# Optimization experiments

Hardware: AMD Instinct MI355X
Metric: run time of the kernel (lower is better)

Reference implementation:

```python
import jax, jax.numpy as jnp
import numpy as np

N_BINS = 256
HOP = 80


def _gru(xs, Wih, Whh, bih, bhh, reverse=False):
    """Single-layer unidirectional GRU, PyTorch gate layout (r, z, n).
    xs: (T, B, I); Wih: (3H, I); Whh: (3H, H). Returns (T, B, H)."""
    H = Whh.shape[1]
    gi = jnp.einsum('tbi,gi->tbg', xs, Wih) + bih  # precompute input projections

    def step(h, gi_t):
        gh = h @ Whh.T + bhh
        ir, iz, inn = jnp.split(gi_t, 3, axis=-1)
        hr, hz, hn = jnp.split(gh, 3, axis=-1)
        r = jax.nn.sigmoid(ir + hr)
        z = jax.nn.sigmoid(iz + hz)
        n = jnp.tanh(inn + r * hn)
        h_new = (1.0 - z) * n + z * h
        return h_new, h_new

    h0 = jnp.zeros((xs.shape[1], H), xs.dtype)
    _, ys = jax.lax.scan(step, h0, gi, reverse=reverse)
    return ys


def _quantize(w):
    # continuous [-1, 1] -> bin index in [0, N_BINS-1]
    return jnp.clip(jnp.floor((w + 1.0) * (N_BINS / 2)), 0, N_BINS - 1).astype(jnp.int32)


def _forward(x, y, p):
    # --- encode: 2-layer bidirectional GRU over mel frames ---
    c = x
    for l in ('m0', 'm1'):
        f = _gru(c, p[l + 'f_Wih'], p[l + 'f_Whh'], p[l + 'f_bih'], p[l + 'f_bhh'])
        bwd = _gru(c, p[l + 'b_Wih'], p[l + 'b_Whh'], p[l + 'b_bih'], p[l + 'b_bhh'], reverse=True)
        c = jnp.concatenate([f, bwd], axis=-1)  # (t_m, b, 2*dim_enc)
    # nearest-neighbor upsample in time (matches F.interpolate default 'nearest')
    c = jnp.repeat(c, HOP, axis=0)  # (t_w, b, 2*dim_enc)

    # --- teacher forcing: shift waveform right, vectorize via embedding ---
    b = x.shape[1]
    w = jnp.concatenate([jnp.zeros((1, b), y.dtype), y[:-1]], axis=0)
    e = p['E'][_quantize(w)]  # (t_w, b, dim_vec)

    # --- wav GRU + projection + GELU ---
    o = _gru(jnp.concatenate([e, c], axis=-1), p['w_Wih'], p['w_Whh'], p['w_bih'], p['w_bhh'])
    o = jax.nn.gelu(o @ p['Wp'].T + p['bp'], approximate=False)  # (t_w, b, dim_proj)

    # --- categorical neg log prob over quantized targets ---
    logits = o @ p['Wd'].T + p['bd']  # (t_w, b, N_BINS)
    logp = jax.nn.log_softmax(logits, axis=-1)
    tgt = _quantize(y)
    nll = -jnp.mean(jnp.take_along_axis(logp, tgt[..., None], axis=-1))
    return nll


def setup_inputs() -> dict:
    key = jax.random.key(0)
    ks = iter(jax.random.split(key, 64))

    def rn(shape, s=0.08):
        return jax.random.normal(next(ks), shape, jnp.float32) * s

    t_m, b, dm = 32, 4, 80
    de, dv, dd, dp = 128, 256, 896, 512
    d = {}
    d['x'] = jax.random.normal(next(ks), (t_m, b, dm), jnp.float32)
    d['y'] = jax.random.uniform(next(ks), (t_m * HOP, b), jnp.float32, minval=-1.0, maxval=1.0)
    for name, i in [('m0f', dm), ('m0b', dm), ('m1f', 2 * de), ('m1b', 2 * de)]:
        d[name + '_Wih'] = rn((3 * de, i))
        d[name + '_Whh'] = rn((3 * de, de))
        d[name + '_bih'] = rn((3 * de,))
        d[name + '_bhh'] = rn((3 * de,))
    d['w_Wih'] = rn((3 * dd, 2 * de + dv))
    d['w_Whh'] = rn((3 * dd, dd))
    d['w_bih'] = rn((3 * dd,))
    d['w_bhh'] = rn((3 * dd,))
    d['Wp'] = rn((dp, dd))
    d['bp'] = rn((dp,))
    d['E'] = rn((N_BINS, dv))
    d['Wd'] = rn((N_BINS, dp))
    d['bd'] = rn((N_BINS,))
    return d


def reference(x, y, m0f_Wih, m0f_Whh, m0f_bih, m0f_bhh, m0b_Wih, m0b_Whh, m0b_bih, m0b_bhh,
              m1f_Wih, m1f_Whh, m1f_bih, m1f_bhh, m1b_Wih, m1b_Whh, m1b_bih, m1b_bhh,
              w_Wih, w_Whh, w_bih, w_bhh, Wp, bp, E, Wd, bd):
    p = dict(m0f_Wih=m0f_Wih, m0f_Whh=m0f_Whh, m0f_bih=m0f_bih, m0f_bhh=m0f_bhh,
             m0b_Wih=m0b_Wih, m0b_Whh=m0b_Whh, m0b_bih=m0b_bih, m0b_bhh=m0b_bhh,
             m1f_Wih=m1f_Wih, m1f_Whh=m1f_Whh, m1f_bih=m1f_bih, m1f_bhh=m1f_bhh,
             m1b_Wih=m1b_Wih, m1b_Whh=m1b_Whh, m1b_bih=m1b_bih, m1b_bhh=m1b_bhh,
             w_Wih=w_Wih, w_Whh=w_Whh, w_bih=w_bih, w_bhh=w_bhh,
             Wp=Wp, bp=bp, E=E, Wd=Wd, bd=bd)
    return _forward(x, y, p)
```

## Files before the change

### kernel.cpp

```cpp
#include <hip/hip_runtime.h>
#include <stdint.h>
#include <math.h>

typedef __attribute__((ext_vector_type(8))) short bf16x8;
typedef __attribute__((ext_vector_type(4))) float f32x4;
typedef __attribute__((ext_vector_type(4))) unsigned int u32x4;

#define BATCH 4
#define T_M 32
#define DE 128
#define T_W 2560
#define NWG 56

__device__ __forceinline__ float b2f(unsigned short h) {
  return __uint_as_float(((unsigned int)h) << 16);
}
__device__ __forceinline__ unsigned short f2b(float f) {
  unsigned int u = __float_as_uint(f);
  u = u + 0x7fffu + ((u >> 16) & 1u);
  return (unsigned short)(u >> 16);
}
__device__ __forceinline__ float blo(unsigned int u){ return __uint_as_float(u << 16); }
__device__ __forceinline__ float bhi(unsigned int u){ return __uint_as_float(u & 0xffff0000u); }
__device__ __forceinline__ float sigm(float x){
  return __builtin_amdgcn_rcpf(1.f + __expf(-x));
}
__device__ __forceinline__ float tanh_fast(float x){
  float x2 = fminf(fmaxf(x + x, -30.f), 30.f);
  return 1.f - 2.f * __builtin_amdgcn_rcpf(__expf(x2) + 1.f);
}
__device__ __forceinline__ float gelu_exact(float x){ return 0.5f * x * (1.f + erff(x * 0.70710678118654752f)); }

__global__ __launch_bounds__(256) void k_prep(
    const float* __restrict__ wih, const float* __restrict__ wp,
    const float* __restrict__ wd, const float* __restrict__ e,
    const float* __restrict__ whh,
    unsigned short* __restrict__ wih_b, unsigned short* __restrict__ wp_b,
    unsigned short* __restrict__ wd_b, unsigned short* __restrict__ eb,
    unsigned short* __restrict__ whh_p)
{
  int idx = blockIdx.x * 256 + threadIdx.x;
  const int N0 = 2688 * 512, N1 = 512 * 896, N2 = 256 * 512, N3 = 256 * 256;
  if (idx < N0) { wih_b[idx] = f2b(wih[idx]); return; }
  idx -= N0;
  if (idx < N1) { wp_b[idx] = f2b(wp[idx]); return; }
  idx -= N1;
  if (idx < N2) { wd_b[idx] = f2b(wd[idx]); return; }
  idx -= N2;
  if (idx < N3) { eb[idx] = f2b(e[idx]); return; }
  idx -= N3;
  if (idx >= 224 * 28 * 512) return;
  int j    = idx & 7;
  int r16  = (idx >> 3) & 15;
  int quad = (idx >> 7) & 3;
  int kc   = (idx >> 9) % 28;
  int G    = (idx >> 9) / 28;
  unsigned short val = 0;
  if (r16 < 12) {
    int row = (r16 >> 2) * 896 + G * 4 + (r16 & 3);
    int col = kc * 32 + quad * 8 + j;
    val = f2b(whh[(size_t)row * 896 + col]);
  }
  whh_p[idx] = val;
}

__global__ __launch_bounds__(384) void k_gi_enc(
    const float* __restrict__ in, const float* __restrict__ Wih,
    const float* __restrict__ bih, float* __restrict__ out, int K)
{
  __shared__ float in_s[256];
  int tb = blockIdx.x;
  for (int i = threadIdx.x; i < K; i += 384) in_s[i] = in[tb * K + i];
  __syncthreads();
  int row = threadIdx.x;
  float acc = bih[row];
  const float* wr = Wih + row * K;
  for (int k = 0; k < K; k += 4) {
    float4 w = *(const float4*)(wr + k);
    float4 v = *(const float4*)(in_s + k);
    acc += w.x * v.x + w.y * v.y + w.z * v.z + w.w * v.w;
  }
  out[tb * 384 + row] = acc;
}

__global__ __launch_bounds__(512) void k_scan_enc(
    const float* __restrict__ gi_f, const float* __restrict__ gi_b,
    const float* __restrict__ whh_f, const float* __restrict__ bhh_f,
    const float* __restrict__ whh_b, const float* __restrict__ bhh_b,
    float* __restrict__ c_out, unsigned short* __restrict__ cb)
{
  const int dir = blockIdx.x, tid = threadIdx.x;
  const float* gi  = dir ? gi_b  : gi_f;
  const float* whh = dir ? whh_b : whh_f;
  const float* bhh = dir ? bhh_b : bhh_f;
  __shared__ unsigned short h_s[BATCH][DE + 8];
  __shared__ float gh_s[384][4];
  __shared__ float bhh_s[384];
  for (int i = tid; i < 384; i += 512) bhh_s[i] = bhh[i];
  for (int i = tid; i < BATCH * (DE + 8); i += 512) ((unsigned short*)h_s)[i] = 0;
  __syncthreads();
  for (int s = 0; s < T_M; ++s) {
    int t = dir ? (T_M - 1 - s) : s;
    #pragma unroll
    for (int k3 = 0; k3 < 3; ++k3) {
      int d = tid + 512 * k3;
      int row = d >> 2, b = d & 3;
      const float* wr = whh + row * DE;
      float acc = 0.f;
      for (int j = 0; j < DE; j += 8) {
        float4 w0 = *(const float4*)(wr + j);
        float4 w1 = *(const float4*)(wr + j + 4);
        uint4  hv = *(const uint4*)&h_s[b][j];
        acc += w0.x * blo(hv.x) + w0.y * bhi(hv.x) + w0.z * blo(hv.y) + w0.w * bhi(hv.y);
        acc += w1.x * blo(hv.z) + w1.y * bhi(hv.z) + w1.z * blo(hv.w) + w1.w * bhi(hv.w);
      }
      gh_s[row][b] = acc + bhh_s[row];
    }
    __syncthreads();
    {
      int u = tid >> 2, b = tid & 3;
      const float* git = gi + (t * BATCH + b) * 384;
      float r = sigm(git[u] + gh_s[u][b]);
      float z = sigm(git[DE + u] + gh_s[DE + u][b]);
      float n = tanh_fast(git[2 * DE + u] + r * gh_s[2 * DE + u][b]);
      float hold = b2f(h_s[b][u]);
      float hnew = (1.f - z) * n + z * hold;
      int oi = (t * BATCH + b) * 256 + dir * DE + u;
      c_out[oi] = hnew;
      if (cb) cb[oi] = f2b(hnew);
      h_s[b][u] = f2b(hnew);
    }
    __syncthreads();
  }
}

__global__ __launch_bounds__(256) void k_mgemm(
    const unsigned short* __restrict__ A, const unsigned short* __restrict__ B,
    const float* __restrict__ bias, void* __restrict__ C,
    int M, int N, int K, int act, int c_bf16, int swz, int afuse,
    const unsigned short* __restrict__ Eb, const unsigned short* __restrict__ c1b,
    const float* __restrict__ yw)
{
  __shared__ unsigned short As[128][40];
  __shared__ unsigned short Bs[128][40];
  const int tid = threadIdx.x;
  const int m0 = blockIdx.x * 128, n0 = blockIdx.y * 128;
  const int lane = tid & 63, wave = tid >> 6;
  const int wy = wave >> 1, wx = wave & 1;
  const int row16 = lane & 15, quad = lane >> 4;
  const int sr = tid >> 1, sc = (tid & 1) * 16;
  const unsigned short* arow0 = nullptr;
  const unsigned short* arow1 = nullptr;
  if (afuse) {
    int row = m0 + sr, tt = row >> 2, b = row & 3;
    float w = (tt == 0) ? 0.f : yw[(tt - 1) * 4 + b];
    int q = (int)floorf((w + 1.f) * 128.f);
    q = q < 0 ? 0 : (q > 255 ? 255 : q);
    arow0 = Eb + q * 256;
    arow1 = c1b + ((tt / 80) * 4 + b) * 256;
  }
  f32x4 acc[4][4] = {};
  for (int kt = 0; kt < K; kt += 32) {
    uint4 av, av2;
    if (afuse) {
      int kk = kt + sc;
      const unsigned short* src = (kk < 256) ? (arow0 + kk) : (arow1 + kk - 256);
      av  = *(const uint4*)src;
      av2 = *(const uint4*)(src + 8);
    } else {
      av  = *(const uint4*)(A + (size_t)(m0 + sr) * K + kt + sc);
      av2 = *(const uint4*)(A + (size_t)(m0 + sr) * K + kt + sc + 8);
    }
    uint4 bv  = *(const uint4*)(B + (size_t)(n0 + sr) * K + kt + sc);
    uint4 bv2 = *(const uint4*)(B + (size_t)(n0 + sr) * K + kt + sc + 8);
    __syncthreads();
    *(uint4*)&As[sr][sc] = av; *(uint4*)&As[sr][sc + 8] = av2;
    *(uint4*)&Bs[sr][sc] = bv; *(uint4*)&Bs[sr][sc + 8] = bv2;
    __syncthreads();
    bf16x8 af[4], bf[4];
    #pragma unroll
    for (int i = 0; i < 4; ++i) af[i] = *(const bf16x8*)&As[wy * 64 + i * 16 + row16][quad * 8];
    #pragma unroll
    for (int j = 0; j < 4; ++j) bf[j] = *(const bf16x8*)&Bs[wx * 64 + j * 16 + row16][quad * 8];
    #pragma unroll
    for (int i = 0; i < 4; ++i)
      #pragma unroll
      for (int j = 0; j < 4; ++j)
        acc[i][j] = __builtin_amdgcn_mfma_f32_16x16x32_bf16(af[i], bf[j], acc[i][j], 0, 0, 0);
  }
  #pragma unroll
  for (int i = 0; i < 4; ++i) {
    #pragma unroll
    for (int j = 0; j < 4; ++j) {
      int col = n0 + wx * 64 + j * 16 + row16;
      float bs = bias[col];
      #pragma unroll
      for (int r = 0; r < 4; ++r) {
        int row = m0 + wy * 64 + i * 16 + quad * 4 + r;
        float v = acc[i][j][r] + bs;
        if (act) v = gelu_exact(v);
        if (swz) {
          int t = row >> 2, b = row & 3;
          int g = col / 896, rem = col - g * 896;
          int G = rem >> 2, u = rem & 3;
          ((unsigned short*)C)[(size_t)(t * 224 + G) * 48 + g * 16 + b * 4 + u] = f2b(v);
        } else if (c_bf16) {
          ((unsigned short*)C)[(size_t)row * N + col] = f2b(v);
        } else {
          ((float*)C)[(size_t)row * N + col] = v;
        }
      }
    }
  }
}

__global__ __launch_bounds__(256, 1) void k_wav_rnn(
    const unsigned short* __restrict__ whh_p,
    const float* __restrict__ bhh,
    const unsigned short* __restrict__ gp_,
    unsigned int* __restrict__ hslots,
    unsigned int* __restrict__ O32)
{
  const int wg = blockIdx.x, tid = threadIdx.x;
  const int lane = tid & 63, wave = tid >> 6;
  const int G = wg * 4 + wave;

  __shared__ unsigned short h_lds[2][4][912];
  __shared__ float phh[4][3][4][4];

  const int r16 = lane & 15, quad = lane >> 4, bb = lane & 3;
  const int fu = (lane >> 2) & 3, fb = lane & 3;

  bf16x8 wf[28];
  {
    const bf16x8* W8 = (const bf16x8*)whh_p + (size_t)G * 28 * 64;
    #pragma unroll
    for (int kc = 0; kc < 28; ++kc)
      wf[kc] = W8[(kc * 4 + quad) * 16 + r16];
  }

  const float br_ = bhh[G * 4 + fu];
  const float bz_ = bhh[896 + G * 4 + fu];
  const float bn_ = bhh[1792 + G * 4 + fu];
  float hprev = 0.f;
  const unsigned short* gl0 = gp_ + (size_t)G * 48 + fb * 4 + fu;
  unsigned short cr = gl0[0], cz = gl0[16], cn = gl0[32];

  const int p0 = tid, p1 = tid + 256, p2 = tid + 512;
  const int p3 = (tid < 128) ? tid + 768 : tid;
  const int pb0 = p0 / 224, pG0 = p0 - pb0 * 224;
  const int pb1 = p1 / 224, pG1 = p1 - pb1 * 224;
  const int pb2 = p2 / 224, pG2 = p2 - pb2 * 224;
  const int pb3 = p3 / 224, pG3 = p3 - pb3 * 224;

  const unsigned long long base0 = (unsigned long long)hslots;
  const unsigned long long base1 = base0 + 14336ull;

  for (int t = 0; t < T_W; ++t) {
    const unsigned long long hb = (t & 1) ? base1 : base0;
    unsigned long long a0 = hb + ((unsigned long long)p0 << 4);
    unsigned long long a1 = hb + ((unsigned long long)p1 << 4);
    unsigned long long a2 = hb + ((unsigned long long)p2 << 4);
    unsigned long long a3 = hb + ((unsigned long long)p3 << 4);
    u32x4 s0, s1, s2, s3;
    const unsigned int tg = (unsigned int)t;
    for (;;) {
      asm volatile(
        "global_load_dwordx4 %0, %4, off sc0 sc1\n"
        "global_load_dwordx4 %1, %5, off sc0 sc1\n"
        "global_load_dwordx4 %2, %6, off sc0 sc1\n"
        "global_load_dwordx4 %3, %7, off sc0 sc1\n"
        "s_waitcnt vmcnt(0)"
        : "=&v"(s0), "=&v"(s1), "=&v"(s2), "=&v"(s3)
        : "v"(a0), "v"(a1), "v"(a2), "v"(a3)
        : "memory");
      unsigned int bad = (s0.z ^ tg) | (s1.z ^ tg) | (s2.z ^ tg) | (s3.z ^ tg);
      if (!__any(bad != 0)) break;
    }

    int tn = (t + 1 < T_W) ? (t + 1) : t;
    const unsigned short* gp = gp_ + (size_t)tn * 10752 + G * 48 + fb * 4 + fu;
    unsigned short nr_ = gp[0], nz_ = gp[16], nn_ = gp[32];

    *(uint2*)&h_lds[t & 1][pb0][pG0 * 4] = make_uint2(s0.x, s0.y);
    *(uint2*)&h_lds[t & 1][pb1][pG1 * 4] = make_uint2(s1.x, s1.y);
    *(uint2*)&h_lds[t & 1][pb2][pG2 * 4] = make_uint2(s2.x, s2.y);
    *(uint2*)&h_lds[t & 1][pb3][pG3 * 4] = make_uint2(s3.x, s3.y);
    __syncthreads();

    f32x4 ac0 = {}, ac1 = {}, ac2 = {}, ac3 = {};
    #pragma unroll
    for (int kc = 0; kc < 28; kc += 4) {
      bf16x8 h0 = *(const bf16x8*)&h_lds[t & 1][bb][(kc + 0) * 32 + quad * 8];
      bf16x8 h1 = *(const bf16x8*)&h_lds[t & 1][bb][(kc + 1) * 32 + quad * 8];
      bf16x8 h2 = *(const bf16x8*)&h_lds[t & 1][bb][(kc + 2) * 32 + quad * 8];
      bf16x8 h3 = *(const bf16x8*)&h_lds[t & 1][bb][(kc + 3) * 32 + quad * 8];
      ac0 = __builtin_amdgcn_mfma_f32_16x16x32_bf16(wf[kc + 0], h0, ac0, 0, 0, 0);
      ac1 = __builtin_amdgcn_mfma_f32_16x16x32_bf16(wf[kc + 1], h1, ac1, 0, 0, 0);
      ac2 = __builtin_amdgcn_mfma_f32_16x16x32_bf16(wf[kc + 2], h2, ac2, 0, 0, 0);
      ac3 = __builtin_amdgcn_mfma_f32_16x16x32_bf16(wf[kc + 3], h3, ac3, 0, 0, 0);
    }
    f32x4 ac;
    ac[0] = ac0[0] + ac1[0] + ac2[0] + ac3[0];
    ac[1] = ac0[1] + ac1[1] + ac2[1] + ac3[1];
    ac[2] = ac0[2] + ac1[2] + ac2[2] + ac3[2];
    ac[3] = ac0[3] + ac1[3] + ac2[3] + ac3[3];

    if (r16 < 4 && quad < 3)
      *(f32x4*)&phh[wave][quad][r16][0] = ac;
    asm volatile("s_waitcnt lgkmcnt(0)" ::: "memory");

    float pr = phh[wave][0][fb][fu];
    float pz = phh[wave][1][fb][fu];
    float pn = phh[wave][2][fb][fu];
    float r = sigm(b2f(cr) + br_ + pr);
    float z = sigm(b2f(cz) + bz_ + pz);
    float n = tanh_fast(b2f(cn) + bn_ + r * pn);
    float h = (1.f - z) * n + z * hprev;
    hprev = h;
    unsigned int hu = f2b(h);
    cr = nr_; cz = nz_; cn = nn_;

    int b = lane & 3;
    unsigned int u0v = (unsigned int)__shfl((int)hu, 0 + b);
    unsigned int u1v = (unsigned int)__shfl((int)hu, 4 + b);
    unsigned int u2v = (unsigned int)__shfl((int)hu, 8 + b);
    unsigned int u3v = (unsigned int)__shfl((int)hu, 12 + b);
    if (lane < 4) {
      u32x4 pkt;
      pkt.x = (u0v & 0xffffu) | (u1v << 16);
      pkt.y = (u2v & 0xffffu) | (u3v << 16);
      pkt.z = (unsigned int)(t + 1);
      pkt.w = 0u;
      unsigned long long sa = (((t + 1) & 1) ? base1 : base0)
                            + (unsigned long long)((b * 224 + G) << 4);
      asm volatile("global_store_dwordx4 %0, %1, off sc0 sc1"
                   :: "v"(sa), "v"(pkt) : "memory");
      *(uint2*)(O32 + (size_t)(t * 4 + b) * 448 + G * 2) = make_uint2(pkt.x, pkt.y);
    }
  }
}

__global__ __launch_bounds__(256) void k_nll(
    const float* __restrict__ logits, const float* __restrict__ y,
    float* __restrict__ partials)
{
  __shared__ float ps[4];
  int wid = threadIdx.x >> 6, lane = threadIdx.x & 63;
  int row = blockIdx.x * 4 + wid;
  const float* lr = logits + (size_t)row * 256;
  float v0 = lr[lane], v1 = lr[lane + 64], v2 = lr[lane + 128], v3 = lr[lane + 192];
  float mx = fmaxf(fmaxf(v0, v1), fmaxf(v2, v3));
  for (int off = 32; off > 0; off >>= 1) mx = fmaxf(mx, __shfl_xor(mx, off));
  float se = __expf(v0 - mx) + __expf(v1 - mx) + __expf(v2 - mx) + __expf(v3 - mx);
  for (int off = 32; off > 0; off >>= 1) se += __shfl_xor(se, off);
  if (lane == 0) {
    float w = y[row];
    int q = (int)floorf((w + 1.f) * 128.f);
    q = q < 0 ? 0 : (q > 255 ? 255 : q);
    ps[wid] = (logf(se) + mx) - lr[q];
  }
  __syncthreads();
  if (threadIdx.x == 0) partials[blockIdx.x] = ps[0] + ps[1] + ps[2] + ps[3];
}

__global__ __launch_bounds__(256) void k_final(const float* __restrict__ partials,
                                               float* __restrict__ out)
{
  __shared__ float s[4];
  int tid = threadIdx.x;
  float a = 0.f;
  for (int i = tid; i < 2560; i += 256) a += partials[i];
  for (int off = 32; off > 0; off >>= 1) a += __shfl_xor(a, off);
  if ((tid & 63) == 0) s[tid >> 6] = a;
  __syncthreads();
  if (tid == 0) out[0] = (s[0] + s[1] + s[2] + s[3]) * (1.f / 10240.f);
}

extern "C" void kernel_launch(void* const* d_in, const int* in_sizes, int n_in,
                              void* d_out, int out_size, void* d_ws, size_t ws_size,
                              hipStream_t stream)
{
  const float* x       = (const float*)d_in[0];
  const float* y       = (const float*)d_in[1];
  const float* m0f_Wih = (const float*)d_in[2];
  const float* m0f_Whh = (const float*)d_in[3];
  const float* m0f_bih = (const float*)d_in[4];
  const float* m0f_bhh = (const float*)d_in[5];
  const float* m0b_Wih = (const float*)d_in[6];
  const float* m0b_Whh = (const float*)d_in[7];
  const float* m0b_bih = (const float*)d_in[8];
  const float* m0b_bhh = (const float*)d_in[9];
  const float* m1f_Wih = (const float*)d_in[10];
  const float* m1f_Whh = (const float*)d_in[11];
  const float* m1f_bih = (const float*)d_in[12];
  const float* m1f_bhh = (const float*)d_in[13];
  const float* m1b_Wih = (const float*)d_in[14];
  const float* m1b_Whh = (const float*)d_in[15];
  const float* m1b_bih = (const float*)d_in[16];
  const float* m1b_bhh = (const float*)d_in[17];
  const float* w_Wih   = (const float*)d_in[18];
  const float* w_Whh   = (const float*)d_in[19];
  const float* w_bih   = (const float*)d_in[20];
  const float* w_bhh   = (const float*)d_in[21];
  const float* Wp      = (const float*)d_in[22];
  const float* bp      = (const float*)d_in[23];
  const float* E       = (const float*)d_in[24];
  const float* Wd      = (const float*)d_in[25];
  const float* bd      = (const float*)d_in[26];

  char* ws = (char*)d_ws;
  size_t off = 0;
  auto alloc = [&](size_t bytes) -> void* {
    void* p = ws + off;
    off += (bytes + 255) & ~(size_t)255;
    return p;
  };
  unsigned int* hslots = (unsigned int*)alloc(2 * 896 * 16);
  size_t misc_bytes = off;

  float* c0   = (float*)alloc((size_t)32 * 4 * 256 * 4);
  float* c1   = (float*)alloc((size_t)32 * 4 * 256 * 4);
  float* gi0f = (float*)alloc((size_t)32 * 4 * 384 * 4);
  float* gi0b = (float*)alloc((size_t)32 * 4 * 384 * 4);
  float* gi1f = (float*)alloc((size_t)32 * 4 * 384 * 4);
  float* gi1b = (float*)alloc((size_t)32 * 4 * 384 * 4);
  unsigned short* Eb    = (unsigned short*)alloc((size_t)256 * 256 * 2);
  unsigned short* c1b   = (unsigned short*)alloc((size_t)32 * 4 * 256 * 2);
  unsigned short* gpack = (unsigned short*)alloc((size_t)2560 * 224 * 48 * 2);
  unsigned int*   O32   = (unsigned int*)alloc((size_t)10240 * 448 * 4);
  unsigned short* O2    = (unsigned short*)alloc((size_t)10240 * 512 * 2);
  float*          LG    = (float*)alloc((size_t)10240 * 256 * 4);
  float*          PT    = (float*)alloc((size_t)2560 * 4);
  unsigned short* Wih_b = (unsigned short*)alloc((size_t)2688 * 512 * 2);
  unsigned short* Whh_p = (unsigned short*)alloc((size_t)224 * 28 * 512 * 2);
  unsigned short* Wp_b  = (unsigned short*)alloc((size_t)512 * 896 * 2);
  unsigned short* Wd_b  = (unsigned short*)alloc((size_t)256 * 512 * 2);

  hipMemsetAsync(d_ws, 0, misc_bytes, stream);

  {
    int total = 2688 * 512 + 512 * 896 + 256 * 512 + 256 * 256 + 224 * 28 * 512;
    k_prep<<<(total + 255) / 256, 256, 0, stream>>>(
        w_Wih, Wp, Wd, E, w_Whh, Wih_b, Wp_b, Wd_b, Eb, Whh_p);
  }

  k_gi_enc<<<128, 384, 0, stream>>>(x, m0f_Wih, m0f_bih, gi0f, 80);
  k_gi_enc<<<128, 384, 0, stream>>>(x, m0b_Wih, m0b_bih, gi0b, 80);
  k_scan_enc<<<2, 512, 0, stream>>>(gi0f, gi0b, m0f_Whh, m0f_bhh, m0b_Whh, m0b_bhh,
                                    c0, nullptr);
  k_gi_enc<<<128, 384, 0, stream>>>(c0, m1f_Wih, m1f_bih, gi1f, 256);
  k_gi_enc<<<128, 384, 0, stream>>>(c0, m1b_Wih, m1b_bih, gi1b, 256);
  k_scan_enc<<<2, 512, 0, stream>>>(gi1f, gi1b, m1f_Whh, m1f_bhh, m1b_Whh, m1b_bhh,
                                    c1, c1b);

  k_mgemm<<<dim3(80, 21), 256, 0, stream>>>(nullptr, Wih_b, w_bih, (void*)gpack,
                                            10240, 2688, 512, 0, 1, 1, 1, Eb, c1b, y);

  k_wav_rnn<<<NWG, 256, 0, stream>>>(Whh_p, w_bhh, gpack, hslots, O32);

  k_mgemm<<<dim3(80, 4), 256, 0, stream>>>((const unsigned short*)O32, Wp_b, bp,
                                           (void*)O2, 10240, 512, 896, 1, 1, 0, 0,
                                           nullptr, nullptr, nullptr);
  k_mgemm<<<dim3(80, 2), 256, 0, stream>>>(O2, Wd_b, bd, (void*)LG,
                                           10240, 256, 512, 0, 0, 0, 0,
                                           nullptr, nullptr, nullptr);
  k_nll<<<2560, 256, 0, stream>>>(LG, y, PT);
  k_final<<<1, 256, 0, stream>>>(PT, (float*)d_out);
}
```

Baseline: 5.777 ms.

## Co-locate wav GRU workgroups on one XCD and exchange hidden state via L2

The recurrent wav GRU kernel now launches 448 workgroups. Each reads its XCC id and uses atomic counters to elect the first XCD that gathers 56 workgroups; all other workgroups exit. The chosen 56 exchange the hidden state through sc0-only (L2-coherent, non-system-scope) loads and stores plus per-wave epoch flags, replacing the sc0 sc1 tagged-packet polling. If election or polling times out, it falls back to the original cross-XCD protocol. Separately, the encoder scan makes each thread compute one weight row for all four batches, reusing the weight loads. This adds launch overhead and relies on the hardware-register and placement assumptions holding.

```diff
diff --git a/kernel.cpp b/kernel.cpp
--- a/kernel.cpp
+++ b/kernel.cpp
@@ -10,7 +10,8 @@
 #define T_M 32
 #define DE 128
 #define T_W 2560
-#define NWG 56
+#define NWG 448
+#define POLL_LIM 4096
 
 __device__ __forceinline__ float b2f(unsigned short h) {
   return __uint_as_float(((unsigned int)h) << 16);
@@ -101,20 +102,27 @@
   __syncthreads();
   for (int s = 0; s < T_M; ++s) {
     int t = dir ? (T_M - 1 - s) : s;
-    #pragma unroll
-    for (int k3 = 0; k3 < 3; ++k3) {
-      int d = tid + 512 * k3;
-      int row = d >> 2, b = d & 3;
-      const float* wr = whh + row * DE;
-      float acc = 0.f;
+    if (tid < 384) {
+      const float* wr = whh + tid * DE;
+      float a0 = 0.f, a1 = 0.f, a2 = 0.f, a3 = 0.f;
       for (int j = 0; j < DE; j += 8) {
         float4 w0 = *(const float4*)(wr + j);
         float4 w1 = *(const float4*)(wr + j + 4);
-        uint4  hv = *(const uint4*)&h_s[b][j];
-        acc += w0.x * blo(hv.x) + w0.y * bhi(hv.x) + w0.z * blo(hv.y) + w0.w * bhi(hv.y);
-        acc += w1.x * blo(hv.z) + w1.y * bhi(hv.z) + w1.z * blo(hv.w) + w1.w * bhi(hv.w);
-      }
-      gh_s[row][b] = acc + bhh_s[row];
+        uint4 h0 = *(const uint4*)&h_s[0][j];
+        uint4 h1 = *(const uint4*)&h_s[1][j];
+        uint4 h2 = *(const uint4*)&h_s[2][j];
+        uint4 h3 = *(const uint4*)&h_s[3][j];
+        a0 += w0.x * blo(h0.x) + w0.y * bhi(h0.x) + w0.z * blo(h0.y) + w0.w * bhi(h0.y);
+        a0 += w1.x * blo(h0.z) + w1.y * bhi(h0.z) + w1.z * blo(h0.w) + w1.w * bhi(h0.w);
+        a1 += w0.x * blo(h1.x) + w0.y * bhi(h1.x) + w0.z * blo(h1.y) + w0.w * bhi(h1.y);
+        a1 += w1.x * blo(h1.z) + w1.y * bhi(h1.z) + w1.z * blo(h1.w) + w1.w * bhi(h1.w);
+        a2 += w0.x * blo(h2.x) + w0.y * bhi(h2.x) + w0.z * blo(h2.y) + w0.w * bhi(h2.y);
+        a2 += w1.x * blo(h2.z) + w1.y * bhi(h2.z) + w1.z * blo(h2.w) + w1.w * bhi(h2.w);
+        a3 += w0.x * blo(h3.x) + w0.y * bhi(h3.x) + w0.z * blo(h3.y) + w0.w * bhi(h3.y);
+        a3 += w1.x * blo(h3.z) + w1.y * bhi(h3.z) + w1.z * blo(h3.w) + w1.w * bhi(h3.w);
+      }
+      float bb_ = bhh_s[tid];
+      *(float4*)&gh_s[tid][0] = make_float4(a0 + bb_, a1 + bb_, a2 + bb_, a3 + bb_);
     }
     __syncthreads();
     {
@@ -214,15 +222,42 @@
   }
 }
 
-__global__ __launch_bounds__(256, 1) void k_wav_rnn(
+__global__ __launch_bounds__(256, 2) void k_wav_rnn(
     const unsigned short* __restrict__ whh_p,
     const float* __restrict__ bhh,
     const unsigned short* __restrict__ gp_,
-    unsigned int* __restrict__ hslots,
+    int* __restrict__ ctl,
+    unsigned short* __restrict__ hLd,
+    int* __restrict__ hLe,
+    unsigned int* __restrict__ hG,
     unsigned int* __restrict__ O32)
 {
-  const int wg = blockIdx.x, tid = threadIdx.x;
+  const int tid = threadIdx.x;
   const int lane = tid & 63, wave = tid >> 6;
+
+  __shared__ int s_wg, s_mode;
+
+  int xcc;
+  asm volatile("s_getreg_b32 %0, hwreg(HW_REG_XCC_ID)" : "=s"(xcc));
+  xcc &= 7;
+  if (tid == 0) {
+    int rank = atomicAdd(&ctl[xcc], 1);
+    if (rank == 55) atomicCAS(&ctl[8], 0, xcc + 1);
+    int w, tries = 0;
+    for (;;) {
+      asm volatile("global_load_dword %0, %1, off sc0 sc1\ns_waitcnt vmcnt(0)"
+                   : "=v"(w) : "v"((unsigned long long)&ctl[8]) : "memory");
+      if (w) break;
+      if (++tries > 20000) atomicCAS(&ctl[8], 0, 15);
+    }
+    if (w == 15) { s_mode = 1; s_wg = blockIdx.x; }
+    else         { s_mode = 0; s_wg = (xcc == w - 1) ? rank : 999; }
+  }
+  __syncthreads();
+  const int fmode = s_mode;
+  const int wg = s_wg;
+  if (wg >= 56) return;
+
   const int G = wg * 4 + wave;
 
   __shared__ unsigned short h_lds[2][4][912];
@@ -246,55 +281,84 @@
   const unsigned short* gl0 = gp_ + (size_t)G * 48 + fb * 4 + fu;
   unsigned short cr = gl0[0], cz = gl0[16], cn = gl0[32];
 
-  const int p0 = tid, p1 = tid + 256, p2 = tid + 512;
-  const int p3 = (tid < 128) ? tid + 768 : tid;
-  const int pb0 = p0 / 224, pG0 = p0 - pb0 * 224;
-  const int pb1 = p1 / 224, pG1 = p1 - pb1 * 224;
-  const int pb2 = p2 / 224, pG2 = p2 - pb2 * 224;
-  const int pb3 = p3 / 224, pG3 = p3 - pb3 * 224;
-
-  const unsigned long long base0 = (unsigned long long)hslots;
-  const unsigned long long base1 = base0 + 14336ull;
+  const int hasC = (tid < 224);
+  const int c0 = hasC ? tid : 0;
+  const int c1 = hasC ? tid + 224 : 0;
+  const int b0 = c0 / 112, k0 = c0 % 112;
+  const int b1 = c1 / 112, k1 = c1 % 112;
+
+  const unsigned long long ldB = (unsigned long long)hLd;
+  const unsigned long long geB = (unsigned long long)hLe;
+  const unsigned long long gB  = (unsigned long long)hG;
+  const unsigned long long aE  = geB + (unsigned long long)((lane < 56 ? lane : 55) * 16);
+
+  int use_glob = fmode;
 
   for (int t = 0; t < T_W; ++t) {
-    const unsigned long long hb = (t & 1) ? base1 : base0;
-    unsigned long long a0 = hb + ((unsigned long long)p0 << 4);
-    unsigned long long a1 = hb + ((unsigned long long)p1 << 4);
-    unsigned long long a2 = hb + ((unsigned long long)p2 << 4);
-    unsigned long long a3 = hb + ((unsigned long long)p3 << 4);
-    u32x4 s0, s1, s2, s3;
-    const unsigned int tg = (unsigned int)t;
-    for (;;) {
-      asm volatile(
-        "global_load_dwordx4 %0, %4, off sc0 sc1\n"
-        "global_load_dwordx4 %1, %5, off sc0 sc1\n"
-        "global_load_dwordx4 %2, %6, off sc0 sc1\n"
-        "global_load_dwordx4 %3, %7, off sc0 sc1\n"
-        "s_waitcnt vmcnt(0)"
-        : "=&v"(s0), "=&v"(s1), "=&v"(s2), "=&v"(s3)
-        : "v"(a0), "v"(a1), "v"(a2), "v"(a3)
-        : "memory");
-      unsigned int bad = (s0.z ^ tg) | (s1.z ^ tg) | (s2.z ^ tg) | (s3.z ^ tg);
-      if (!__any(bad != 0)) break;
+    const int par = t & 1;
+
+    if (!use_glob) {
+      int tries = 0;
+      for (;;) {
+        u32x4 e;
+        asm volatile("global_load_dwordx4 %0, %1, off sc0\ns_waitcnt vmcnt(0)"
+                     : "=&v"(e) : "v"(aE) : "memory");
+        int ok = ((int)e.x >= t) && ((int)e.y >= t) && ((int)e.z >= t) && ((int)e.w >= t);
+        if (__all(ok)) break;
+        if (++tries > POLL_LIM) { use_glob = 1; break; }
+      }
+    }
+    if (!use_glob) {
+      if (hasC) {
+        u32x4 d0, d1;
+        unsigned long long aD0 = ldB + (unsigned long long)(par * 7168 + b0 * 1792 + k0 * 16);
+        unsigned long long aD1 = ldB + (unsigned long long)(par * 7168 + b1 * 1792 + k1 * 16);
+        asm volatile("global_load_dwordx4 %0, %2, off sc0\n"
+                     "global_load_dwordx4 %1, %3, off sc0\n"
+                     "s_waitcnt vmcnt(0)"
+                     : "=&v"(d0), "=&v"(d1) : "v"(aD0), "v"(aD1) : "memory");
+        *(u32x4*)((char*)h_lds + par * 7296 + b0 * 1824 + k0 * 16) = d0;
+        *(u32x4*)((char*)h_lds + par * 7296 + b1 * 1824 + k1 * 16) = d1;
+      }
+    } else {
+      if (hasC) {
+        unsigned long long aG0 = gB + (unsigned long long)((par * 896 + b0 * 224 + 2 * k0) * 16);
+        unsigned long long aG2 = gB + (unsigned long long)((par * 896 + b1 * 224 + 2 * k1) * 16);
+        u32x4 g0, g1, g2, g3;
+        const unsigned int tg = (unsigned int)t;
+        for (;;) {
+          asm volatile("global_load_dwordx4 %0, %4, off sc0 sc1\n"
+                       "global_load_dwordx4 %1, %5, off sc0 sc1\n"
+                       "global_load_dwordx4 %2, %6, off sc0 sc1\n"
+                       "global_load_dwordx4 %3, %7, off sc0 sc1\n"
+                       "s_waitcnt vmcnt(0)"
+                       : "=&v"(g0), "=&v"(g1), "=&v"(g2), "=&v"(g3)
+                       : "v"(aG0), "v"(aG0 + 16), "v"(aG2), "v"(aG2 + 16)
+                       : "memory");
+          unsigned int bad = (g0.z ^ tg) | (g1.z ^ tg) | (g2.z ^ tg) | (g3.z ^ tg);
+          if (!__any(bad != 0)) break;
+        }
+        u32x4 d0, d1;
+        d0.x = g0.x; d0.y = g0.y; d0.z = g1.x; d0.w = g1.y;
+        d1.x = g2.x; d1.y = g2.y; d1.z = g3.x; d1.w = g3.y;
+        *(u32x4*)((char*)h_lds + par * 7296 + b0 * 1824 + k0 * 16) = d0;
+        *(u32x4*)((char*)h_lds + par * 7296 + b1 * 1824 + k1 * 16) = d1;
+      }
     }
 
     int tn = (t + 1 < T_W) ? (t + 1) : t;
     const unsigned short* gp = gp_ + (size_t)tn * 10752 + G * 48 + fb * 4 + fu;
     unsigned short nr_ = gp[0], nz_ = gp[16], nn_ = gp[32];
 
-    *(uint2*)&h_lds[t & 1][pb0][pG0 * 4] = make_uint2(s0.x, s0.y);
-    *(uint2*)&h_lds[t & 1][pb1][pG1 * 4] = make_uint2(s1.x, s1.y);
-    *(uint2*)&h_lds[t & 1][pb2][pG2 * 4] = make_uint2(s2.x, s2.y);
-    *(uint2*)&h_lds[t & 1][pb3][pG3 * 4] = make_uint2(s3.x, s3.y);
     __syncthreads();
 
     f32x4 ac0 = {}, ac1 = {}, ac2 = {}, ac3 = {};
     #pragma unroll
     for (int kc = 0; kc < 28; kc += 4) {
-      bf16x8 h0 = *(const bf16x8*)&h_lds[t & 1][bb][(kc + 0) * 32 + quad * 8];
-      bf16x8 h1 = *(const bf16x8*)&h_lds[t & 1][bb][(kc + 1) * 32 + quad * 8];
-      bf16x8 h2 = *(const bf16x8*)&h_lds[t & 1][bb][(kc + 2) * 32 + quad * 8];
-      bf16x8 h3 = *(const bf16x8*)&h_lds[t & 1][bb][(kc + 3) * 32 + quad * 8];
+      bf16x8 h0 = *(const bf16x8*)&h_lds[par][bb][(kc + 0) * 32 + quad * 8];
+      bf16x8 h1 = *(const bf16x8*)&h_lds[par][bb][(kc + 1) * 32 + quad * 8];
+      bf16x8 h2 = *(const bf16x8*)&h_lds[par][bb][(kc + 2) * 32 + quad * 8];
+      bf16x8 h3 = *(const bf16x8*)&h_lds[par][bb][(kc + 3) * 32 + quad * 8];
       ac0 = __builtin_amdgcn_mfma_f32_16x16x32_bf16(wf[kc + 0], h0, ac0, 0, 0, 0);
       ac1 = __builtin_amdgcn_mfma_f32_16x16x32_bf16(wf[kc + 1], h1, ac1, 0, 0, 0);
       ac2 = __builtin_amdgcn_mfma_f32_16x16x32_bf16(wf[kc + 2], h2, ac2, 0, 0, 0);
@@ -327,16 +391,27 @@
     unsigned int u2v = (unsigned int)__shfl((int)hu, 8 + b);
     unsigned int u3v = (unsigned int)__shfl((int)hu, 12 + b);
     if (lane < 4) {
+      unsigned int lo = (u0v & 0xffffu) | (u1v << 16);
+      unsigned int hi = (u2v & 0xffffu) | (u3v << 16);
+      const int pn2 = (t + 1) & 1;
+      *(uint2*)(O32 + (size_t)(t * 4 + b) * 448 + G * 2) = make_uint2(lo, hi);
+      if (!fmode) {
+        unsigned long long aL = ldB + (unsigned long long)(pn2 * 7168 + b * 1792 + G * 8);
+        uint2 ld2 = make_uint2(lo, hi);
+        asm volatile("global_store_dwordx2 %0, %1, off sc0" :: "v"(aL), "v"(ld2) : "memory");
+      }
       u32x4 pkt;
-      pkt.x = (u0v & 0xffffu) | (u1v << 16);
-      pkt.y = (u2v & 0xffffu) | (u3v << 16);
-      pkt.z = (unsigned int)(t + 1);
-      pkt.w = 0u;
-      unsigned long long sa = (((t + 1) & 1) ? base1 : base0)
-                            + (unsigned long long)((b * 224 + G) << 4);
-      asm volatile("global_store_dwordx4 %0, %1, off sc0 sc1"
-                   :: "v"(sa), "v"(pkt) : "memory");
-      *(uint2*)(O32 + (size_t)(t * 4 + b) * 448 + G * 2) = make_uint2(pkt.x, pkt.y);
+      pkt.x = lo; pkt.y = hi; pkt.z = (unsigned int)(t + 1); pkt.w = 0u;
+      unsigned long long aGp = gB + (unsigned long long)((pn2 * 896 + b * 224 + G) * 16);
+      asm volatile("global_store_dwordx4 %0, %1, off sc0 sc1" :: "v"(aGp), "v"(pkt) : "memory");
+      if (!fmode) {
+        asm volatile("s_waitcnt vmcnt(1)" ::: "memory");
+        if (lane == 0) {
+          unsigned long long aEp = geB + (unsigned long long)((wg * 4 + wave) * 4);
+          int ev = t + 1;
+          asm volatile("global_store_dword %0, %1, off sc0" :: "v"(aEp), "v"(ev) : "memory");
+        }
+      }
     }
   }
 }
@@ -416,7 +491,10 @@
     off += (bytes + 255) & ~(size_t)255;
     return p;
   };
-  unsigned int* hslots = (unsigned int*)alloc(2 * 896 * 16);
+  int*            ctl  = (int*)alloc(16 * 4);
+  unsigned short* hLd  = (unsigned short*)alloc((size_t)2 * 4 * 896 * 2);
+  int*            hLe  = (int*)alloc((size_t)224 * 4);
+  unsigned int*   hG   = (unsigned int*)alloc((size_t)2 * 896 * 16);
   size_t misc_bytes = off;
 
   float* c0   = (float*)alloc((size_t)32 * 4 * 256 * 4);
@@ -457,7 +535,7 @@
   k_mgemm<<<dim3(80, 21), 256, 0, stream>>>(nullptr, Wih_b, w_bih, (void*)gpack,
                                             10240, 2688, 512, 0, 1, 1, 1, Eb, c1b, y);
 
-  k_wav_rnn<<<NWG, 256, 0, stream>>>(Whh_p, w_bhh, gpack, hslots, O32);
+  k_wav_rnn<<<NWG, 256, 0, stream>>>(Whh_p, w_bhh, gpack, ctl, hLd, hLe, hG, O32);
 
   k_mgemm<<<dim3(80, 4), 256, 0, stream>>>((const unsigned short*)O32, Wp_b, bp,
                                            (void*)O2, 10240, 512, 896, 1, 1, 0, 0,
```

Measured after the change: 8.983 ms. 1.56x slower.

## Co-locate wav RNN workgroups on one XCC for L2-local hidden-state exchange

Applied to the files above, without the earlier changes.

The wav GRU launch grows to 448 workgroups, and each one reads its XCC id and counts arrivals. The first XCC to gather 56 workgroups becomes the active set and the rest exit. Those workers exchange hidden state through L2-coherent loads and stores (sc0 only) instead of system-coherent ones, aiming to cut per-step cross-XCC sync latency. A global fallback path with a poll limit and dual stores guards against misplacement, at the cost of extra stores and launch overhead. The encoder scan is also restructured so each thread computes all four batch rows for one weight row, reusing each weight load.

```diff
diff --git a/kernel.cpp b/kernel.cpp
--- a/kernel.cpp
+++ b/kernel.cpp
@@ -10,7 +10,8 @@
 #define T_M 32
 #define DE 128
 #define T_W 2560
-#define NWG 56
+#define NWG 448
+#define POLL_LIM 4096
 
 __device__ __forceinline__ float b2f(unsigned short h) {
   return __uint_as_float(((unsigned int)h) << 16);
@@ -101,20 +102,27 @@
   __syncthreads();
   for (int s = 0; s < T_M; ++s) {
     int t = dir ? (T_M - 1 - s) : s;
-    #pragma unroll
-    for (int k3 = 0; k3 < 3; ++k3) {
-      int d = tid + 512 * k3;
-      int row = d >> 2, b = d & 3;
-      const float* wr = whh + row * DE;
-      float acc = 0.f;
+    if (tid < 384) {
+      const float* wr = whh + tid * DE;
+      float a0 = 0.f, a1 = 0.f, a2 = 0.f, a3 = 0.f;
       for (int j = 0; j < DE; j += 8) {
         float4 w0 = *(const float4*)(wr + j);
         float4 w1 = *(const float4*)(wr + j + 4);
-        uint4  hv = *(const uint4*)&h_s[b][j];
-        acc += w0.x * blo(hv.x) + w0.y * bhi(hv.x) + w0.z * blo(hv.y) + w0.w * bhi(hv.y);
-        acc += w1.x * blo(hv.z) + w1.y * bhi(hv.z) + w1.z * blo(hv.w) + w1.w * bhi(hv.w);
+        uint4 h0 = *(const uint4*)&h_s[0][j];
+        uint4 h1 = *(const uint4*)&h_s[1][j];
+        uint4 h2 = *(const uint4*)&h_s[2][j];
+        uint4 h3 = *(const uint4*)&h_s[3][j];
+        a0 += w0.x * blo(h0.x) + w0.y * bhi(h0.x) + w0.z * blo(h0.y) + w0.w * bhi(h0.y);
+        a0 += w1.x * blo(h0.z) + w1.y * bhi(h0.z) + w1.z * blo(h0.w) + w1.w * bhi(h0.w);
+        a1 += w0.x * blo(h1.x) + w0.y * bhi(h1.x) + w0.z * blo(h1.y) + w0.w * bhi(h1.y);
+        a1 += w1.x * blo(h1.z) + w1.y * bhi(h1.z) + w1.z * blo(h1.w) + w1.w * bhi(h1.w);
+        a2 += w0.x * blo(h2.x) + w0.y * bhi(h2.x) + w0.z * blo(h2.y) + w0.w * bhi(h2.y);
+        a2 += w1.x * blo(h2.z) + w1.y * bhi(h2.z) + w1.z * blo(h2.w) + w1.w * bhi(h2.w);
+        a3 += w0.x * blo(h3.x) + w0.y * bhi(h3.x) + w0.z * blo(h3.y) + w0.w * bhi(h3.y);
+        a3 += w1.x * blo(h3.z) + w1.y * bhi(h3.z) + w1.z * blo(h3.w) + w1.w * bhi(h3.w);
       }
-      gh_s[row][b] = acc + bhh_s[row];
+      float bb_ = bhh_s[tid];
+      *(float4*)&gh_s[tid][0] = make_float4(a0 + bb_, a1 + bb_, a2 + bb_, a3 + bb_);
     }
     __syncthreads();
     {
@@ -214,15 +222,41 @@
   }
 }
 
-__global__ __launch_bounds__(256, 1) void k_wav_rnn(
+__global__ __launch_bounds__(256, 2) void k_wav_rnn(
     const unsigned short* __restrict__ whh_p,
     const float* __restrict__ bhh,
     const unsigned short* __restrict__ gp_,
-    unsigned int* __restrict__ hslots,
+    int* __restrict__ ctl,
+    unsigned int* __restrict__ hloc,
+    unsigned int* __restrict__ hglob,
     unsigned int* __restrict__ O32)
 {
-  const int wg = blockIdx.x, tid = threadIdx.x;
+  const int tid = threadIdx.x;
   const int lane = tid & 63, wave = tid >> 6;
+
+  __shared__ int s_wg, s_mode;
+
+  int xcc;
+  asm volatile("s_getreg_b32 %0, hwreg(HW_REG_XCC_ID)" : "=s"(xcc));
+  xcc &= 7;
+  if (tid == 0) {
+    int rank = atomicAdd(&ctl[xcc], 1);
+    if (rank == 55) atomicCAS(&ctl[8], 0, xcc + 1);
+    int w, tries = 0;
+    for (;;) {
+      asm volatile("global_load_dword %0, %1, off sc0 sc1\ns_waitcnt vmcnt(0)"
+                   : "=v"(w) : "v"((unsigned long long)&ctl[8]) : "memory");
+      if (w) break;
+      if (++tries > 20000) atomicCAS(&ctl[8], 0, 15);
+    }
+    if (w == 15) { s_mode = 1; s_wg = blockIdx.x; }
+    else         { s_mode = 0; s_wg = (xcc == w - 1) ? rank : 999; }
+  }
+  __syncthreads();
+  const int fmode = s_mode;
+  const int wg = s_wg;
+  if (wg >= 56) return;
+
   const int G = wg * 4 + wave;
 
   __shared__ unsigned short h_lds[2][4][912];
@@ -253,29 +287,55 @@
   const int pb2 = p2 / 224, pG2 = p2 - pb2 * 224;
   const int pb3 = p3 / 224, pG3 = p3 - pb3 * 224;
 
-  const unsigned long long base0 = (unsigned long long)hslots;
-  const unsigned long long base1 = base0 + 14336ull;
+  const unsigned long long lb0 = (unsigned long long)hloc;
+  const unsigned long long lb1 = lb0 + 14336ull;
+  const unsigned long long gb0 = (unsigned long long)hglob;
+  const unsigned long long gb1 = gb0 + 14336ull;
+
+  int use_glob = fmode;
 
   for (int t = 0; t < T_W; ++t) {
-    const unsigned long long hb = (t & 1) ? base1 : base0;
+    unsigned long long hb = use_glob ? ((t & 1) ? gb1 : gb0)
+                                     : ((t & 1) ? lb1 : lb0);
     unsigned long long a0 = hb + ((unsigned long long)p0 << 4);
     unsigned long long a1 = hb + ((unsigned long long)p1 << 4);
     unsigned long long a2 = hb + ((unsigned long long)p2 << 4);
     unsigned long long a3 = hb + ((unsigned long long)p3 << 4);
     u32x4 s0, s1, s2, s3;
     const unsigned int tg = (unsigned int)t;
+    int tries = 0;
     for (;;) {
-      asm volatile(
-        "global_load_dwordx4 %0, %4, off sc0 sc1\n"
-        "global_load_dwordx4 %1, %5, off sc0 sc1\n"
-        "global_load_dwordx4 %2, %6, off sc0 sc1\n"
-        "global_load_dwordx4 %3, %7, off sc0 sc1\n"
-        "s_waitcnt vmcnt(0)"
-        : "=&v"(s0), "=&v"(s1), "=&v"(s2), "=&v"(s3)
-        : "v"(a0), "v"(a1), "v"(a2), "v"(a3)
-        : "memory");
+      if (!use_glob) {
+        asm volatile(
+          "global_load_dwordx4 %0, %4, off sc0\n"
+          "global_load_dwordx4 %1, %5, off sc0\n"
+          "global_load_dwordx4 %2, %6, off sc0\n"
+          "global_load_dwordx4 %3, %7, off sc0\n"
+          "s_waitcnt vmcnt(0)"
+          : "=&v"(s0), "=&v"(s1), "=&v"(s2), "=&v"(s3)
+          : "v"(a0), "v"(a1), "v"(a2), "v"(a3)
+          : "memory");
+      } else {
+        asm volatile(
+          "global_load_dwordx4 %0, %4, off sc0 sc1\n"
+          "global_load_dwordx4 %1, %5, off sc0 sc1\n"
+          "global_load_dwordx4 %2, %6, off sc0 sc1\n"
+          "global_load_dwordx4 %3, %7, off sc0 sc1\n"
+          "s_waitcnt vmcnt(0)"
+          : "=&v"(s0), "=&v"(s1), "=&v"(s2), "=&v"(s3)
+          : "v"(a0), "v"(a1), "v"(a2), "v"(a3)
+          : "memory");
+      }
       unsigned int bad = (s0.z ^ tg) | (s1.z ^ tg) | (s2.z ^ tg) | (s3.z ^ tg);
       if (!__any(bad != 0)) break;
+      if (!use_glob && ++tries > POLL_LIM) {
+        use_glob = 1;
+        hb = (t & 1) ? gb1 : gb0;
+        a0 = hb + ((unsigned long long)p0 << 4);
+        a1 = hb + ((unsigned long long)p1 << 4);
+        a2 = hb + ((unsigned long long)p2 << 4);
+        a3 = hb + ((unsigned long long)p3 << 4);
+      }
     }
 
     int tn = (t + 1 < T_W) ? (t + 1) : t;
@@ -332,10 +392,16 @@
       pkt.y = (u2v & 0xffffu) | (u3v << 16);
       pkt.z = (unsigned int)(t + 1);
       pkt.w = 0u;
-      unsigned long long sa = (((t + 1) & 1) ? base1 : base0)
-                            + (unsigned long long)((b * 224 + G) << 4);
+      const unsigned long long off4 = (unsigned long long)((b * 224 + G) << 4);
+      const int par = (t + 1) & 1;
+      if (!fmode) {
+        unsigned long long sl = (par ? lb1 : lb0) + off4;
+        asm volatile("global_store_dwordx4 %0, %1, off sc0"
+                     :: "v"(sl), "v"(pkt) : "memory");
+      }
+      unsigned long long sg = (par ? gb1 : gb0) + off4;
       asm volatile("global_store_dwordx4 %0, %1, off sc0 sc1"
-                   :: "v"(sa), "v"(pkt) : "memory");
+                   :: "v"(sg), "v"(pkt) : "memory");
       *(uint2*)(O32 + (size_t)(t * 4 + b) * 448 + G * 2) = make_uint2(pkt.x, pkt.y);
     }
   }
@@ -416,7 +482,9 @@
     off += (bytes + 255) & ~(size_t)255;
     return p;
   };
-  unsigned int* hslots = (unsigned int*)alloc(2 * 896 * 16);
+  int*          ctl   = (int*)alloc(16 * 4);
+  unsigned int* hloc  = (unsigned int*)alloc((size_t)2 * 896 * 16);
+  unsigned int* hglob = (unsigned int*)alloc((size_t)2 * 896 * 16);
   size_t misc_bytes = off;
 
   float* c0   = (float*)alloc((size_t)32 * 4 * 256 * 4);
@@ -457,7 +525,7 @@
   k_mgemm<<<dim3(80, 21), 256, 0, stream>>>(nullptr, Wih_b, w_bih, (void*)gpack,
                                             10240, 2688, 512, 0, 1, 1, 1, Eb, c1b, y);
 
-  k_wav_rnn<<<NWG, 256, 0, stream>>>(Whh_p, w_bhh, gpack, hslots, O32);
+  k_wav_rnn<<<NWG, 256, 0, stream>>>(Whh_p, w_bhh, gpack, ctl, hloc, hglob, O32);
 
   k_mgemm<<<dim3(80, 4), 256, 0, stream>>>((const unsigned short*)O32, Wp_b, bp,
                                            (void*)O2, 10240, 512, 896, 1, 1, 0, 0,
```

Result: slower. 7.847 ms (+35.8%).
